# Kernel optimization log

Hardware: AMD Instinct MI355X
Metric: run time of the kernel (lower is better)

## Reference

```python
import jax, jax.numpy as jnp
import numpy as np

B, S, D = 2, 2048, 1024
H = 16
HD = D // H  # head dim 64


def setup_inputs() -> dict:
    key = jax.random.key(0)
    ks = jax.random.split(key, 7)
    queries = jax.random.normal(ks[0], (B, S, D), dtype=jnp.float32)
    keys = jax.random.normal(ks[1], (B, S, D), dtype=jnp.float32)
    values = jax.random.normal(ks[2], (B, S, D), dtype=jnp.float32)
    scale = 1.0 / np.sqrt(D)
    Wq = jax.random.normal(ks[3], (D, D), dtype=jnp.float32) * scale
    Wk = jax.random.normal(ks[4], (D, D), dtype=jnp.float32) * scale
    Wv = jax.random.normal(ks[5], (D, D), dtype=jnp.float32) * scale
    Wo = jax.random.normal(ks[6], (D, D), dtype=jnp.float32) * scale
    return {"queries": queries, "keys": keys, "values": values,
            "Wq": Wq, "Wk": Wk, "Wv": Wv, "Wo": Wo}


def _split_heads(x):
    # [B,S,D] -> [B,H,S,HD]
    b, s, d = x.shape
    return x.reshape(b, s, H, d // H).transpose(0, 2, 1, 3)


def reference(queries, keys, values, Wq, Wk, Wv, Wo):
    q = _split_heads(queries @ Wq) * (HD ** -0.5)   # [B,H,S,HD]
    k = _split_heads(keys @ Wk)
    v = _split_heads(values @ Wv)
    logits = jnp.einsum('bhqd,bhkd->bhqk', q, k)     # [B,H,S,S]
    weights = jax.nn.softmax(logits, axis=-1)
    ctx = jnp.einsum('bhqk,bhkd->bhqd', weights, v)  # [B,H,S,HD]
    ctx = ctx.transpose(0, 2, 1, 3).reshape(B, S, D)
    return ctx @ Wo
```

## Files before the change

### kernel.cpp

```cpp
#include <hip/hip_runtime.h>
#include <hip/hip_bf16.h>


typedef short s16x8 __attribute__((ext_vector_type(8)));
typedef float f32x4v __attribute__((ext_vector_type(4)));
typedef float f32x16v __attribute__((ext_vector_type(16)));
typedef unsigned int u32x4v __attribute__((ext_vector_type(4)));

__device__ inline unsigned short f2bf(float f) {
    union { float f; unsigned int i; } x; x.f = f;
    unsigned int r = x.i + 0x7FFFu + ((x.i >> 16) & 1u);
    return (unsigned short)(r >> 16);
}
__device__ inline unsigned int pkbf(float lo, float hi) {
    return (unsigned int)f2bf(lo) | ((unsigned int)f2bf(hi) << 16);
}

__device__ inline void gld_lds16(const unsigned short* g, unsigned short* l) {
    __builtin_amdgcn_global_load_lds(
        (const __attribute__((address_space(1))) unsigned int*)(const void*)g,
        (__attribute__((address_space(3))) unsigned int*)(void*)l,
        16, 0, 0);
}

__global__ __launch_bounds__(256)
void cvt3(const float* __restrict__ W0, const float* __restrict__ W1, const float* __restrict__ W2,
          unsigned short* __restrict__ T0, unsigned short* __restrict__ T1, unsigned short* __restrict__ T2) {
    const float* W = (blockIdx.z == 0) ? W0 : (blockIdx.z == 1) ? W1 : W2;
    unsigned short* Wt = (blockIdx.z == 0) ? T0 : (blockIdx.z == 1) ? T1 : T2;
    __shared__ __align__(16) unsigned short Ls[64 * 72];
    const int t = threadIdx.x;
    const int k0 = blockIdx.y * 64, n0 = blockIdx.x * 64;
    const int r = t >> 4, c4 = (t & 15) * 4;
    #pragma unroll
    for (int i = 0; i < 4; ++i) {
        float4 wv = *(const float4*)&W[(size_t)(k0 + r + i * 16) * 1024 + n0 + c4];
        Ls[(c4 + 0) * 72 + r + i * 16] = f2bf(wv.x);
        Ls[(c4 + 1) * 72 + r + i * 16] = f2bf(wv.y);
        Ls[(c4 + 2) * 72 + r + i * 16] = f2bf(wv.z);
        Ls[(c4 + 3) * 72 + r + i * 16] = f2bf(wv.w);
    }
    __syncthreads();
    #pragma unroll
    for (int i = 0; i < 2; ++i) {
        const int p = i * 256 + t;
        const int n = p & 63, kc = p >> 6;
        s16x8 v = *(const s16x8*)&Ls[n * 72 + kc * 8];
        const int gn = n0 + n, k = k0 + kc * 8;
        const size_t g = ((size_t)(gn >> 7) * 128 + (k >> 3)) * 128 + (gn & 127);
        *(s16x8*)&Wt[g * 8] = v;
    }
}

__global__ __launch_bounds__(256)
void cvtA(const float* __restrict__ A0, const float* __restrict__ A1, const float* __restrict__ A2,
          unsigned short* __restrict__ O0, unsigned short* __restrict__ O1, unsigned short* __restrict__ O2) {
    const float* A = (blockIdx.z == 0) ? A0 : (blockIdx.z == 1) ? A1 : A2;
    unsigned short* O = (blockIdx.z == 0) ? O0 : (blockIdx.z == 1) ? O1 : O2;
    __shared__ __align__(16) unsigned short Ls[8192];
    const int t = threadIdx.x;
    const int k0 = blockIdx.x * 64, rp = blockIdx.y;
    const int row = t >> 1, kh = (t & 1) * 32;
    const float* src = A + (size_t)(rp * 128 + row) * 1024 + k0 + kh;
    float4 f[8];
    #pragma unroll
    for (int i = 0; i < 8; ++i) f[i] = ((const float4*)src)[i];
    #pragma unroll
    for (int j = 0; j < 4; ++j) {
        uint4 u;
        u.x = pkbf(f[j * 2].x, f[j * 2].y);
        u.y = pkbf(f[j * 2].z, f[j * 2].w);
        u.z = pkbf(f[j * 2 + 1].x, f[j * 2 + 1].y);
        u.w = pkbf(f[j * 2 + 1].z, f[j * 2 + 1].w);
        const int kc = (t & 1) * 4 + j;
        *(uint4*)&Ls[(kc * 128 + row) * 8] = u;
    }
    __syncthreads();
    const size_t gbase = ((size_t)rp * 128 + (k0 >> 3)) * 128;
    #pragma unroll
    for (int i = 0; i < 4; ++i) {
        const int idx = i * 256 + t;
        *(uint4*)&O[(gbase + idx) * 8] = *(const uint4*)&Ls[idx * 8];
    }
}

__global__ __launch_bounds__(256, 3)
void gemm_qkv(const unsigned short* __restrict__ Aq, const unsigned short* __restrict__ Ak,
              const unsigned short* __restrict__ Av,
              const unsigned short* __restrict__ W0, const unsigned short* __restrict__ W1,
              const unsigned short* __restrict__ W2,
              unsigned short* __restrict__ OQ, unsigned short* __restrict__ OK,
              unsigned short* __restrict__ OV, float scaleQ) {
    const int p = blockIdx.x;
    const int L = (p & 7) * 96 + (p >> 3);
    const int z = L >> 8;
    const int rem = L & 255;
    const int m0 = (rem >> 3) * 128, n0 = (rem & 7) * 128;
    const unsigned short* Asw = (z == 0) ? Aq : (z == 1) ? Ak : Av;
    const unsigned short* Bsw = (z == 0) ? W0 : (z == 1) ? W1 : W2;
    const float scale = (z == 0) ? scaleQ : 1.0f;

    __shared__ __align__(16) unsigned short Al[2][4096];
    __shared__ __align__(16) unsigned short Bl[2][4096];
    const int t = threadIdx.x, lane = t & 63, w = t >> 6;
    const int ln = lane & 15, qd = lane >> 4;
    const int mw = (w & 1) * 64, nw = (w >> 1) * 64;
    const size_t gaB = (size_t)(m0 >> 7) * 16384;
    const size_t gbB = (size_t)(n0 >> 7) * 16384;

    f32x4v acc[4][4] = {};

    auto stage = [&](int kt, int b) {
        const size_t ga = gaB + (size_t)kt * 512;
        const size_t gb = gbB + (size_t)kt * 512;
        #pragma unroll
        for (int j = 0; j < 2; ++j)
            gld_lds16(Asw + (ga + j * 256 + t) * 8, &Al[b][(j * 256 + w * 64) * 8]);
        #pragma unroll
        for (int j = 0; j < 2; ++j)
            gld_lds16(Bsw + (gb + j * 256 + t) * 8, &Bl[b][(j * 256 + w * 64) * 8]);
    };

    stage(0, 0);
    stage(1, 1);
    for (int kt = 0; kt < 32; ++kt) {
        if (kt < 31) asm volatile("s_waitcnt vmcnt(4)" ::: "memory");
        else         asm volatile("s_waitcnt vmcnt(0)" ::: "memory");
        __builtin_amdgcn_s_barrier();
        asm volatile("" ::: "memory");
        const int b = kt & 1;
        {
            s16x8 a[4], bb[4];
            #pragma unroll
            for (int mt = 0; mt < 4; ++mt)
                a[mt] = *(const s16x8*)&Al[b][(qd * 128 + mw + mt * 16 + ln) * 8];
            #pragma unroll
            for (int nt = 0; nt < 4; ++nt)
                bb[nt] = *(const s16x8*)&Bl[b][(qd * 128 + nw + nt * 16 + ln) * 8];
            #pragma unroll
            for (int mt = 0; mt < 4; ++mt)
                #pragma unroll
                for (int nt = 0; nt < 4; ++nt)
                    acc[mt][nt] = __builtin_amdgcn_mfma_f32_16x16x32_bf16(a[mt], bb[nt], acc[mt][nt], 0, 0, 0);
        }
        if (kt < 30) {
            __builtin_amdgcn_s_barrier();
            asm volatile("" ::: "memory");
            stage(kt + 2, b);
        }
    }

    #pragma unroll
    for (int mt = 0; mt < 4; ++mt)
        #pragma unroll
        for (int nt = 0; nt < 4; ++nt)
            #pragma unroll
            for (int i = 0; i < 4; ++i) {
                const int m = m0 + mw + mt * 16 + qd * 4 + i;
                const int n = n0 + nw + nt * 16 + ln;
                const float v = acc[mt][nt][i] * scale;
                const int bh = (m >> 11) * 16 + (n >> 6), s = m & 2047, hd = n & 63;
                if (z == 0) {
                    OQ[((size_t)bh * 2048 + s) * 64 + hd] = f2bf(v);
                } else if (z == 1) {
                    const size_t g = ((size_t)(bh * 32 + (s >> 6)) * 8 + (hd >> 3)) * 64 + (s & 63);
                    OK[g * 8 + (hd & 7)] = f2bf(v);
                } else {
                    const size_t g = ((size_t)(bh * 32 + (s >> 6)) * 8 + ((s >> 3) & 7)) * 64 + hd;
                    OV[g * 8 + (s & 7)] = f2bf(v);
                }
            }
}

__global__ __launch_bounds__(256, 3)
void gemm_qkv_pack(const float* __restrict__ A0, const float* __restrict__ A1, const float* __restrict__ A2,
                   const unsigned short* __restrict__ W0, const unsigned short* __restrict__ W1,
                   const unsigned short* __restrict__ W2,
                   unsigned short* __restrict__ OQ, unsigned short* __restrict__ OK,
                   unsigned short* __restrict__ OV, float scaleQ) {
    const int z = blockIdx.z;
    const float* Avv = (z == 0) ? A0 : (z == 1) ? A1 : A2;
    const unsigned short* Bsw = (z == 0) ? W0 : (z == 1) ? W1 : W2;
    const float scale = (z == 0) ? scaleQ : 1.0f;

    __shared__ __align__(16) unsigned short Al[1024 * 8];
    __shared__ __align__(16) unsigned short Bl[1024 * 8];
    const int t = threadIdx.x;
    const int lane = t & 63, w = t >> 6;
    const int ln = lane & 15, qd = lane >> 4;
    const int mw = (w & 1) * 64, nw = (w >> 1) * 64;
    const int m0 = blockIdx.y * 128, n0 = blockIdx.x * 128;

    f32x4v acc[4][4] = {};

    for (int k0 = 0; k0 < 1024; k0 += 64) {
        __syncthreads();
        {
            const size_t gb = ((size_t)(n0 >> 7) * 128 + (k0 >> 3)) * 128;
            #pragma unroll
            for (int j = 0; j < 4; ++j)
                gld_lds16(Bsw + (gb + j * 256 + t) * 8, &Bl[(j * 256 + w * 64) * 8]);
        }
        #pragma unroll
        for (int j = 0; j < 4; ++j) {
            const int pp = j * 256 + t;
            const int row = pp >> 3, kc = pp & 7;
            const float* src = Avv + (size_t)(m0 + row) * 1024 + k0 + kc * 8;
            float4 f0 = ((const float4*)src)[0];
            float4 f1 = ((const float4*)src)[1];
            uint4 u;
            u.x = pkbf(f0.x, f0.y); u.y = pkbf(f0.z, f0.w);
            u.z = pkbf(f1.x, f1.y); u.w = pkbf(f1.z, f1.w);
            *(uint4*)&Al[(kc * 128 + (row ^ kc)) * 8] = u;
        }
        __syncthreads();

        #pragma unroll
        for (int kk = 0; kk < 2; ++kk) {
            const int kc = kk * 4 + qd;
            s16x8 a[4], b[4];
            #pragma unroll
            for (int mt = 0; mt < 4; ++mt)
                a[mt] = *(const s16x8*)&Al[(kc * 128 + ((mw + mt * 16 + ln) ^ kc)) * 8];
            #pragma unroll
            for (int nt = 0; nt < 4; ++nt)
                b[nt] = *(const s16x8*)&Bl[(kc * 128 + nw + nt * 16 + ln) * 8];
            #pragma unroll
            for (int mt = 0; mt < 4; ++mt)
                #pragma unroll
                for (int nt = 0; nt < 4; ++nt)
                    acc[mt][nt] = __builtin_amdgcn_mfma_f32_16x16x32_bf16(a[mt], b[nt], acc[mt][nt], 0, 0, 0);
        }
    }

    #pragma unroll
    for (int mt = 0; mt < 4; ++mt)
        #pragma unroll
        for (int nt = 0; nt < 4; ++nt)
            #pragma unroll
            for (int i = 0; i < 4; ++i) {
                const int m = m0 + mw + mt * 16 + qd * 4 + i;
                const int n = n0 + nw + nt * 16 + ln;
                const float v = acc[mt][nt][i] * scale;
                const int bh = (m >> 11) * 16 + (n >> 6), s = m & 2047, hd = n & 63;
                if (z == 0) {
                    OQ[((size_t)bh * 2048 + s) * 64 + hd] = f2bf(v);
                } else if (z == 1) {
                    const size_t g = ((size_t)(bh * 32 + (s >> 6)) * 8 + (hd >> 3)) * 64 + (s & 63);
                    OK[g * 8 + (hd & 7)] = f2bf(v);
                } else {
                    const size_t g = ((size_t)(bh * 32 + (s >> 6)) * 8 + ((s >> 3) & 7)) * 64 + hd;
                    OV[g * 8 + (s & 7)] = f2bf(v);
                }
            }
}

__global__ __launch_bounds__(256, 2)
void gemm_out(const unsigned short* __restrict__ Asw, const unsigned short* __restrict__ Bsw,
              float* __restrict__ outF) {
    const int p = blockIdx.x;
    const int L = (p & 7) * 64 + (p >> 3);
    const int m0 = (L >> 4) * 128, n0 = (L & 15) * 64;

    __shared__ __align__(16) unsigned short Al[2][8192];
    __shared__ __align__(16) unsigned short Bl[2][4096];
    const int t = threadIdx.x, lane = t & 63, w = t >> 6;
    const int ln = lane & 15, qd = lane >> 4;
    const int mw = (w & 1) * 64, nw = (w >> 1) * 32;
    const size_t gaB = (size_t)(m0 >> 7) * 16384;
    const size_t gbB = (size_t)(n0 >> 7) * 16384 + (n0 & 127);

    f32x4v acc[4][2] = {};

    auto stage = [&](int kt, int b) {
        const size_t ga = gaB + (size_t)kt * 1024;
        #pragma unroll
        for (int j = 0; j < 4; ++j)
            gld_lds16(Asw + (ga + j * 256 + t) * 8, &Al[b][(j * 256 + w * 64) * 8]);
        #pragma unroll
        for (int i = 0; i < 2; ++i) {
            const int c = w * 2 + i;
            const size_t gb = gbB + (size_t)(kt * 8 + c) * 128 + lane;
            gld_lds16(Bsw + gb * 8, &Bl[b][(c * 64) * 8]);
        }
    };

    stage(0, 0);
    stage(1, 1);
    for (int kt = 0; kt < 16; ++kt) {
        if (kt < 15) asm volatile("s_waitcnt vmcnt(6)" ::: "memory");
        else         asm volatile("s_waitcnt vmcnt(0)" ::: "memory");
        __builtin_amdgcn_s_barrier();
        asm volatile("" ::: "memory");
        const int b = kt & 1;
        #pragma unroll
        for (int kk = 0; kk < 2; ++kk) {
            const int kc = kk * 4 + qd;
            s16x8 a[4], bb[2];
            #pragma unroll
            for (int mt = 0; mt < 4; ++mt)
                a[mt] = *(const s16x8*)&Al[b][(kc * 128 + mw + mt * 16 + ln) * 8];
            #pragma unroll
            for (int nt = 0; nt < 2; ++nt)
                bb[nt] = *(const s16x8*)&Bl[b][(kc * 64 + nw + nt * 16 + ln) * 8];
            #pragma unroll
            for (int mt = 0; mt < 4; ++mt)
                #pragma unroll
                for (int nt = 0; nt < 2; ++nt)
                    acc[mt][nt] = __builtin_amdgcn_mfma_f32_16x16x32_bf16(a[mt], bb[nt], acc[mt][nt], 0, 0, 0);
        }
        if (kt < 14) {
            __builtin_amdgcn_s_barrier();
            asm volatile("" ::: "memory");
            stage(kt + 2, b);
        }
    }

    #pragma unroll
    for (int mt = 0; mt < 4; ++mt)
        #pragma unroll
        for (int nt = 0; nt < 2; ++nt)
            #pragma unroll
            for (int i = 0; i < 4; ++i) {
                const int m = m0 + mw + mt * 16 + qd * 4 + i;
                const int n = n0 + nw + nt * 16 + ln;
                outF[(size_t)m * 1024 + n] = acc[mt][nt][i];
            }
}

__device__ __forceinline__ void fa_compute(
        const unsigned short* Ksb, const unsigned short* Vsb,
        const int H, const int l31, const s16x8* qf,
        f32x16v* accO, float& ls0, float& ls1, float& ls2, float& ls3) {
    f32x16v accS[2] = {};
    #pragma unroll
    for (int kk = 0; kk < 4; ++kk) {
        s16x8 kf0 = *(const s16x8*)&Ksb[((kk * 2 + H) * 64 + l31) * 8];
        s16x8 kf1 = *(const s16x8*)&Ksb[((kk * 2 + H) * 64 + 32 + l31) * 8];
        accS[0] = __builtin_amdgcn_mfma_f32_32x32x16_bf16(kf0, qf[kk], accS[0], 0, 0, 0);
        accS[1] = __builtin_amdgcn_mfma_f32_32x32x16_bf16(kf1, qf[kk], accS[1], 0, 0, 0);
    }

    u32x4v af[4];
    #pragma unroll
    for (int mt = 0; mt < 2; ++mt) {
        float p[16];
        #pragma unroll
        for (int r = 0; r < 16; ++r)
            p[r] = exp2f(accS[mt][r]);
        #pragma unroll
        for (int r = 0; r < 16; r += 4) {
            ls0 += p[r + 0]; ls1 += p[r + 1]; ls2 += p[r + 2]; ls3 += p[r + 3];
        }
        unsigned int C[8];
        #pragma unroll
        for (int j = 0; j < 8; ++j)
            asm("v_cvt_pk_bf16_f32 %0, %1, %2" : "=v"(C[j]) : "v"(p[2 * j]), "v"(p[2 * j + 1]));
        #pragma unroll
        for (int pp = 0; pp < 2; ++pp) {
            unsigned int x0 = C[4 * pp + 0], y0 = C[4 * pp + 2];
            unsigned int x1 = C[4 * pp + 1], y1 = C[4 * pp + 3];
            asm("v_permlane32_swap_b32 %0, %1" : "+v"(x0), "+v"(y0));
            asm("v_permlane32_swap_b32 %0, %1" : "+v"(x1), "+v"(y1));
            u32x4v a; a.x = x0; a.y = x1; a.z = y0; a.w = y1;
            af[mt * 2 + pp] = a;
        }
    }

    #pragma unroll
    for (int kk2 = 0; kk2 < 4; ++kk2) {
        s16x8 a = __builtin_bit_cast(s16x8, af[kk2]);
        s16x8 vf0 = *(const s16x8*)&Vsb[((kk2 * 2 + H) * 64 + l31) * 8];
        s16x8 vf1 = *(const s16x8*)&Vsb[((kk2 * 2 + H) * 64 + 32 + l31) * 8];
        accO[0] = __builtin_amdgcn_mfma_f32_32x32x16_bf16(a, vf0, accO[0], 0, 0, 0);
        accO[1] = __builtin_amdgcn_mfma_f32_32x32x16_bf16(a, vf1, accO[1], 0, 0, 0);
    }
}

__global__ __launch_bounds__(256, 2)
void fattn(const unsigned short* __restrict__ Q, const unsigned short* __restrict__ Ksw,
           const unsigned short* __restrict__ Vsw, unsigned short* __restrict__ ctx) {
    __shared__ __align__(16) unsigned short Ks3[3][512 * 8];
    __shared__ __align__(16) unsigned short Vs3[3][512 * 8];

    const int t = threadIdx.x, lane = t & 63, w = t >> 6;
    const int l31 = lane & 31, H = lane >> 5;
    const int bid = blockIdx.x + (blockIdx.y << 4);
    const int wid = (bid & 7) * 64 + (bid >> 3);
    const int bh = wid >> 4, m0 = (wid & 15) * 128;
    const size_t head = (size_t)bh * 2048 * 64;

    s16x8 qf[4];
    #pragma unroll
    for (int kk = 0; kk < 4; ++kk)
        qf[kk] = *(const s16x8*)(Q + head + (size_t)(m0 + w * 32 + l31) * 64 + kk * 16 + H * 8);
    asm volatile("s_waitcnt vmcnt(0)" ::: "memory");
    #pragma unroll
    for (int kk = 0; kk < 4; ++kk) {
        u32x4v q = __builtin_bit_cast(u32x4v, qf[kk]);
        asm volatile("" : "+v"(q.x), "+v"(q.y), "+v"(q.z), "+v"(q.w));
        qf[kk] = __builtin_bit_cast(s16x8, q);
    }

    const size_t tb = (size_t)bh * 32 * 512;
    {
        #pragma unroll
        for (int kt = 0; kt < 2; ++kt)
            #pragma unroll
            for (int j = 0; j < 2; ++j) {
                gld_lds16(Ksw + (tb + kt * 512 + j * 256 + t) * 8, &Ks3[kt][(j * 256 + w * 64) * 8]);
                gld_lds16(Vsw + (tb + kt * 512 + j * 256 + t) * 8, &Vs3[kt][(j * 256 + w * 64) * 8]);
            }
    }

    f32x16v accO[2] = {};
    float ls0 = 0.f, ls1 = 0.f, ls2 = 0.f, ls3 = 0.f;

    int cur = 0;
    for (int kt = 0; kt < 31; ++kt) {
        asm volatile("s_waitcnt vmcnt(4)" ::: "memory");
        __builtin_amdgcn_s_barrier();
        asm volatile("" ::: "memory");
        if (kt < 30) {
            const int ib = (cur == 0) ? 2 : cur - 1;
            const size_t tbn = tb + (size_t)(kt + 2) * 512;
            #pragma unroll
            for (int j = 0; j < 2; ++j) {
                gld_lds16(Ksw + (tbn + j * 256 + t) * 8, &Ks3[ib][(j * 256 + w * 64) * 8]);
                gld_lds16(Vsw + (tbn + j * 256 + t) * 8, &Vs3[ib][(j * 256 + w * 64) * 8]);
            }
        }
        fa_compute(Ks3[cur], Vs3[cur], H, l31, qf, accO, ls0, ls1, ls2, ls3);
        cur = (cur == 2) ? 0 : cur + 1;
    }
    asm volatile("s_waitcnt vmcnt(0)" ::: "memory");
    __builtin_amdgcn_s_barrier();
    asm volatile("" ::: "memory");
    fa_compute(Ks3[cur], Vs3[cur], H, l31, qf, accO, ls0, ls1, ls2, ls3);

    float lsum = (ls0 + ls1) + (ls2 + ls3);
    lsum += __shfl_xor(lsum, 32, 64);
    const float inv = 1.f / lsum;

    #pragma unroll
    for (int r = 0; r < 16; ++r) {
        const int qloc = (r & 3) + 8 * (r >> 2) + 4 * H;
        const float rinv = __shfl(inv, qloc, 64);
        const int mrow = (bh >> 4) * 2048 + m0 + w * 32 + qloc;
        #pragma unroll
        for (int nt = 0; nt < 2; ++nt) {
            const int k = (bh & 15) * 64 + nt * 32 + l31;
            const size_t g = ((size_t)(mrow >> 7) * 128 + (k >> 3)) * 128 + (mrow & 127);
            ctx[g * 8 + (k & 7)] = f2bf(accO[nt][r] * rinv);
        }
    }
}

extern "C" void kernel_launch(void* const* d_in, const int* in_sizes, int n_in,
                              void* d_out, int out_size, void* d_ws, size_t ws_size,
                              hipStream_t stream) {
    char* ws = (char*)d_ws;
    unsigned short* Qb  = (unsigned short*)(ws);
    unsigned short* Ksw = (unsigned short*)(ws + ((size_t)8 << 20));
    unsigned short* Vsw = (unsigned short*)(ws + ((size_t)16 << 20));
    unsigned short* Wqt = (unsigned short*)(ws + ((size_t)24 << 20));
    unsigned short* Wkt = (unsigned short*)(ws + ((size_t)26 << 20));
    unsigned short* Wvt = (unsigned short*)(ws + ((size_t)28 << 20));
    unsigned short* Aq  = (unsigned short*)(ws + ((size_t)30 << 20));
    unsigned short* Ak  = (unsigned short*)(ws + ((size_t)38 << 20));
    unsigned short* Av  = (unsigned short*)(ws + ((size_t)46 << 20));
    unsigned short* ctx = (unsigned short*)(ws + ((size_t)24 << 20));
    unsigned short* Wot = (unsigned short*)(ws);

    const bool big = ws_size >= ((size_t)54 << 20);

    cvt3<<<dim3(16, 16, 3), 256, 0, stream>>>((const float*)d_in[3], (const float*)d_in[4],
                                              (const float*)d_in[5], Wqt, Wkt, Wvt);

    if (big) {
        cvtA<<<dim3(16, 32, 3), 256, 0, stream>>>((const float*)d_in[0], (const float*)d_in[1],
                                                  (const float*)d_in[2], Aq, Ak, Av);
        gemm_qkv<<<dim3(768), 256, 0, stream>>>(Aq, Ak, Av, Wqt, Wkt, Wvt,
                                                Qb, Ksw, Vsw, 0.125f * 1.44269504f);
    } else {
        gemm_qkv_pack<<<dim3(8, 32, 3), 256, 0, stream>>>(
            (const float*)d_in[0], (const float*)d_in[1], (const float*)d_in[2],
            Wqt, Wkt, Wvt, Qb, Ksw, Vsw, 0.125f * 1.44269504f);
    }

    fattn<<<dim3(16, 32), dim3(256), 0, stream>>>(Qb, Ksw, Vsw, ctx);

    cvt3<<<dim3(16, 16, 1), 256, 0, stream>>>((const float*)d_in[6], nullptr, nullptr,
                                              Wot, nullptr, nullptr);

    gemm_out<<<dim3(512), 256, 0, stream>>>(ctx, Wot, (float*)d_out);
}
```

Baseline: 233.0 us.

## Split attention over KV halves with combine kernel and MFMA row-sum

```diff
diff --git a/kernel.cpp b/kernel.cpp
--- a/kernel.cpp
+++ b/kernel.cpp
@@ -14,6 +14,9 @@
 }
 __device__ inline unsigned int pkbf(float lo, float hi) {
     return (unsigned int)f2bf(lo) | ((unsigned int)f2bf(hi) << 16);
+}
+__device__ inline float bf2f(unsigned short u) {
+    union { unsigned int i; float f; } x; x.i = (unsigned int)u << 16; return x.f;
 }
 
 __device__ inline void gld_lds16(const unsigned short* g, unsigned short* l) {
@@ -172,89 +175,6 @@
             }
 }
 
-__global__ __launch_bounds__(256, 3)
-void gemm_qkv_pack(const float* __restrict__ A0, const float* __restrict__ A1, const float* __restrict__ A2,
-                   const unsigned short* __restrict__ W0, const unsigned short* __restrict__ W1,
-                   const unsigned short* __restrict__ W2,
-                   unsigned short* __restrict__ OQ, unsigned short* __restrict__ OK,
-                   unsigned short* __restrict__ OV, float scaleQ) {
-    const int z = blockIdx.z;
-    const float* Avv = (z == 0) ? A0 : (z == 1) ? A1 : A2;
-    const unsigned short* Bsw = (z == 0) ? W0 : (z == 1) ? W1 : W2;
-    const float scale = (z == 0) ? scaleQ : 1.0f;
-
-    __shared__ __align__(16) unsigned short Al[1024 * 8];
-    __shared__ __align__(16) unsigned short Bl[1024 * 8];
-    const int t = threadIdx.x;
-    const int lane = t & 63, w = t >> 6;
-    const int ln = lane & 15, qd = lane >> 4;
-    const int mw = (w & 1) * 64, nw = (w >> 1) * 64;
-    const int m0 = blockIdx.y * 128, n0 = blockIdx.x * 128;
-
-    f32x4v acc[4][4] = {};
-
-    for (int k0 = 0; k0 < 1024; k0 += 64) {
-        __syncthreads();
-        {
-            const size_t gb = ((size_t)(n0 >> 7) * 128 + (k0 >> 3)) * 128;
-            #pragma unroll
-            for (int j = 0; j < 4; ++j)
-                gld_lds16(Bsw + (gb + j * 256 + t) * 8, &Bl[(j * 256 + w * 64) * 8]);
-        }
-        #pragma unroll
-        for (int j = 0; j < 4; ++j) {
-            const int pp = j * 256 + t;
-            const int row = pp >> 3, kc = pp & 7;
-            const float* src = Avv + (size_t)(m0 + row) * 1024 + k0 + kc * 8;
-            float4 f0 = ((const float4*)src)[0];
-            float4 f1 = ((const float4*)src)[1];
-            uint4 u;
-            u.x = pkbf(f0.x, f0.y); u.y = pkbf(f0.z, f0.w);
-            u.z = pkbf(f1.x, f1.y); u.w = pkbf(f1.z, f1.w);
-            *(uint4*)&Al[(kc * 128 + (row ^ kc)) * 8] = u;
-        }
-        __syncthreads();
-
-        #pragma unroll
-        for (int kk = 0; kk < 2; ++kk) {
-            const int kc = kk * 4 + qd;
-            s16x8 a[4], b[4];
-            #pragma unroll
-            for (int mt = 0; mt < 4; ++mt)
-                a[mt] = *(const s16x8*)&Al[(kc * 128 + ((mw + mt * 16 + ln) ^ kc)) * 8];
-            #pragma unroll
-            for (int nt = 0; nt < 4; ++nt)
-                b[nt] = *(const s16x8*)&Bl[(kc * 128 + nw + nt * 16 + ln) * 8];
-            #pragma unroll
-            for (int mt = 0; mt < 4; ++mt)
-                #pragma unroll
-                for (int nt = 0; nt < 4; ++nt)
-                    acc[mt][nt] = __builtin_amdgcn_mfma_f32_16x16x32_bf16(a[mt], b[nt], acc[mt][nt], 0, 0, 0);
-        }
-    }
-
-    #pragma unroll
-    for (int mt = 0; mt < 4; ++mt)
-        #pragma unroll
-        for (int nt = 0; nt < 4; ++nt)
-            #pragma unroll
-            for (int i = 0; i < 4; ++i) {
-                const int m = m0 + mw + mt * 16 + qd * 4 + i;
-                const int n = n0 + nw + nt * 16 + ln;
-                const float v = acc[mt][nt][i] * scale;
-                const int bh = (m >> 11) * 16 + (n >> 6), s = m & 2047, hd = n & 63;
-                if (z == 0) {
-                    OQ[((size_t)bh * 2048 + s) * 64 + hd] = f2bf(v);
-                } else if (z == 1) {
-                    const size_t g = ((size_t)(bh * 32 + (s >> 6)) * 8 + (hd >> 3)) * 64 + (s & 63);
-                    OK[g * 8 + (hd & 7)] = f2bf(v);
-                } else {
-                    const size_t g = ((size_t)(bh * 32 + (s >> 6)) * 8 + ((s >> 3) & 7)) * 64 + hd;
-                    OV[g * 8 + (s & 7)] = f2bf(v);
-                }
-            }
-}
-
 __global__ __launch_bounds__(256, 2)
 void gemm_out(const unsigned short* __restrict__ Asw, const unsigned short* __restrict__ Bsw,
               float* __restrict__ outF) {
@@ -331,7 +251,7 @@
 __device__ __forceinline__ void fa_compute(
         const unsigned short* Ksb, const unsigned short* Vsb,
         const int H, const int l31, const s16x8* qf,
-        f32x16v* accO, float& ls0, float& ls1, float& ls2, float& ls3) {
+        f32x16v* accO, f32x16v& accL) {
     f32x16v accS[2] = {};
     #pragma unroll
     for (int kk = 0; kk < 4; ++kk) {
@@ -348,10 +268,6 @@
         #pragma unroll
         for (int r = 0; r < 16; ++r)
             p[r] = exp2f(accS[mt][r]);
-        #pragma unroll
-        for (int r = 0; r < 16; r += 4) {
-            ls0 += p[r + 0]; ls1 += p[r + 1]; ls2 += p[r + 2]; ls3 += p[r + 3];
-        }
         unsigned int C[8];
         #pragma unroll
         for (int j = 0; j < 8; ++j)
@@ -367,6 +283,8 @@
         }
     }
 
+    const s16x8 ones = {(short)0x3F80, (short)0x3F80, (short)0x3F80, (short)0x3F80,
+                        (short)0x3F80, (short)0x3F80, (short)0x3F80, (short)0x3F80};
     #pragma unroll
     for (int kk2 = 0; kk2 < 4; ++kk2) {
         s16x8 a = __builtin_bit_cast(s16x8, af[kk2]);
@@ -374,20 +292,24 @@
         s16x8 vf1 = *(const s16x8*)&Vsb[((kk2 * 2 + H) * 64 + 32 + l31) * 8];
         accO[0] = __builtin_amdgcn_mfma_f32_32x32x16_bf16(a, vf0, accO[0], 0, 0, 0);
         accO[1] = __builtin_amdgcn_mfma_f32_32x32x16_bf16(a, vf1, accO[1], 0, 0, 0);
-    }
-}
-
-__global__ __launch_bounds__(256, 2)
-void fattn(const unsigned short* __restrict__ Q, const unsigned short* __restrict__ Ksw,
-           const unsigned short* __restrict__ Vsw, unsigned short* __restrict__ ctx) {
-    __shared__ __align__(16) unsigned short Ks3[3][512 * 8];
-    __shared__ __align__(16) unsigned short Vs3[3][512 * 8];
+        accL    = __builtin_amdgcn_mfma_f32_32x32x16_bf16(a, ones, accL, 0, 0, 0);
+    }
+}
+
+__global__ __launch_bounds__(256, 4)
+void fattn_sp(const unsigned short* __restrict__ Q, const unsigned short* __restrict__ Ksw,
+              const unsigned short* __restrict__ Vsw, unsigned short* __restrict__ Opart,
+              float* __restrict__ Lpart) {
+    __shared__ __align__(16) unsigned short Ks2[2][4096];
+    __shared__ __align__(16) unsigned short Vs2[2][4096];
 
     const int t = threadIdx.x, lane = t & 63, w = t >> 6;
     const int l31 = lane & 31, H = lane >> 5;
-    const int bid = blockIdx.x + (blockIdx.y << 4);
-    const int wid = (bid & 7) * 64 + (bid >> 3);
-    const int bh = wid >> 4, m0 = (wid & 15) * 128;
+    const int bid = blockIdx.x;
+    const int wid = (bid & 7) * 128 + (bid >> 3);
+    const int bh = wid >> 5, inner = wid & 31;
+    const int split = inner >> 4, mblk = inner & 15;
+    const int m0 = mblk * 128;
     const size_t head = (size_t)bh * 2048 * 64;
 
     s16x8 qf[4];
@@ -402,56 +324,96 @@
         qf[kk] = __builtin_bit_cast(s16x8, q);
     }
 
-    const size_t tb = (size_t)bh * 32 * 512;
-    {
-        #pragma unroll
-        for (int kt = 0; kt < 2; ++kt)
-            #pragma unroll
-            for (int j = 0; j < 2; ++j) {
-                gld_lds16(Ksw + (tb + kt * 512 + j * 256 + t) * 8, &Ks3[kt][(j * 256 + w * 64) * 8]);
-                gld_lds16(Vsw + (tb + kt * 512 + j * 256 + t) * 8, &Vs3[kt][(j * 256 + w * 64) * 8]);
-            }
-    }
+    const size_t tb = (size_t)(bh * 32 + split * 16) * 512;
+    auto stage = [&](int kt, int b) {
+        const size_t tk = tb + (size_t)kt * 512;
+        #pragma unroll
+        for (int j = 0; j < 2; ++j)
+            gld_lds16(Ksw + (tk + j * 256 + t) * 8, &Ks2[b][(j * 256 + w * 64) * 8]);
+        #pragma unroll
+        for (int j = 0; j < 2; ++j)
+            gld_lds16(Vsw + (tk + j * 256 + t) * 8, &Vs2[b][(j * 256 + w * 64) * 8]);
+    };
+
+    stage(0, 0);
+    stage(1, 1);
 
     f32x16v accO[2] = {};
-    float ls0 = 0.f, ls1 = 0.f, ls2 = 0.f, ls3 = 0.f;
-
-    int cur = 0;
-    for (int kt = 0; kt < 31; ++kt) {
-        asm volatile("s_waitcnt vmcnt(4)" ::: "memory");
+    f32x16v accL = {};
+
+    for (int kt = 0; kt < 16; ++kt) {
+        if (kt < 15) asm volatile("s_waitcnt vmcnt(4)" ::: "memory");
+        else         asm volatile("s_waitcnt vmcnt(0)" ::: "memory");
         __builtin_amdgcn_s_barrier();
         asm volatile("" ::: "memory");
-        if (kt < 30) {
-            const int ib = (cur == 0) ? 2 : cur - 1;
-            const size_t tbn = tb + (size_t)(kt + 2) * 512;
-            #pragma unroll
-            for (int j = 0; j < 2; ++j) {
-                gld_lds16(Ksw + (tbn + j * 256 + t) * 8, &Ks3[ib][(j * 256 + w * 64) * 8]);
-                gld_lds16(Vsw + (tbn + j * 256 + t) * 8, &Vs3[ib][(j * 256 + w * 64) * 8]);
-            }
-        }
-        fa_compute(Ks3[cur], Vs3[cur], H, l31, qf, accO, ls0, ls1, ls2, ls3);
-        cur = (cur == 2) ? 0 : cur + 1;
-    }
-    asm volatile("s_waitcnt vmcnt(0)" ::: "memory");
-    __builtin_amdgcn_s_barrier();
-    asm volatile("" ::: "memory");
-    fa_compute(Ks3[cur], Vs3[cur], H, l31, qf, accO, ls0, ls1, ls2, ls3);
-
-    float lsum = (ls0 + ls1) + (ls2 + ls3);
-    lsum += __shfl_xor(lsum, 32, 64);
-    const float inv = 1.f / lsum;
+        fa_compute(Ks2[kt & 1], Vs2[kt & 1], H, l31, qf, accO, accL);
+        if (kt < 14) {
+            __builtin_amdgcn_s_barrier();
+            asm volatile("" ::: "memory");
+            stage(kt + 2, kt & 1);
+        }
+    }
+
+    const int lb = bh * 16 + mblk;
+    unsigned int Wd[16];
+    #pragma unroll
+    for (int nt = 0; nt < 2; ++nt)
+        #pragma unroll
+        for (int r = 0; r < 16; r += 2)
+            Wd[nt * 8 + r / 2] = pkbf(accO[nt][r], accO[nt][r + 1]);
+    uint4* od = (uint4*)(Opart + ((size_t)(split * 512 + lb) * 256 + t) * 32);
+    od[0] = *(const uint4*)&Wd[0];
+    od[1] = *(const uint4*)&Wd[4];
+    od[2] = *(const uint4*)&Wd[8];
+    od[3] = *(const uint4*)&Wd[12];
+    if (l31 == 0) {
+        float lv[16];
+        #pragma unroll
+        for (int r = 0; r < 16; ++r) lv[r] = accL[r];
+        float4* ld = (float4*)(Lpart + (((size_t)(split * 512 + lb) * 4 + w) * 2 + H) * 16);
+        ld[0] = *(const float4*)&lv[0];
+        ld[1] = *(const float4*)&lv[4];
+        ld[2] = *(const float4*)&lv[8];
+        ld[3] = *(const float4*)&lv[12];
+    }
+}
+
+__global__ __launch_bounds__(256)
+void fa_comb(const unsigned short* __restrict__ Opart, const float* __restrict__ Lpart,
+             unsigned short* __restrict__ ctx) {
+    const int lb = blockIdx.x, t = threadIdx.x;
+    const int lane = t & 63, w = t >> 6;
+    const int l31 = lane & 31, H = lane >> 5;
+    const int bh = lb >> 4, m0 = (lb & 15) * 128;
+
+    const float* L0 = Lpart + (((size_t)lb * 4 + w) * 2 + H) * 16;
+    const float* L1 = Lpart + (((size_t)(512 + lb) * 4 + w) * 2 + H) * 16;
+    float inv[16];
+    #pragma unroll
+    for (int r = 0; r < 16; ++r) inv[r] = 1.f / (L0[r] + L1[r]);
+
+    const uint4* o0 = (const uint4*)(Opart + ((size_t)lb * 256 + t) * 32);
+    const uint4* o1 = (const uint4*)(Opart + ((size_t)(512 + lb) * 256 + t) * 32);
+    unsigned int A0[16], A1[16];
+    *(uint4*)&A0[0] = o0[0]; *(uint4*)&A0[4] = o0[1];
+    *(uint4*)&A0[8] = o0[2]; *(uint4*)&A0[12] = o0[3];
+    *(uint4*)&A1[0] = o1[0]; *(uint4*)&A1[4] = o1[1];
+    *(uint4*)&A1[8] = o1[2]; *(uint4*)&A1[12] = o1[3];
 
     #pragma unroll
     for (int r = 0; r < 16; ++r) {
         const int qloc = (r & 3) + 8 * (r >> 2) + 4 * H;
-        const float rinv = __shfl(inv, qloc, 64);
         const int mrow = (bh >> 4) * 2048 + m0 + w * 32 + qloc;
         #pragma unroll
         for (int nt = 0; nt < 2; ++nt) {
+            const int j = nt * 16 + r;
+            const unsigned int w0 = A0[j >> 1], w1 = A1[j >> 1];
+            const unsigned short h0 = (j & 1) ? (unsigned short)(w0 >> 16) : (unsigned short)(w0 & 0xFFFF);
+            const unsigned short h1 = (j & 1) ? (unsigned short)(w1 >> 16) : (unsigned short)(w1 & 0xFFFF);
+            const float out = (bf2f(h0) + bf2f(h1)) * inv[r];
             const int k = (bh & 15) * 64 + nt * 32 + l31;
             const size_t g = ((size_t)(mrow >> 7) * 128 + (k >> 3)) * 128 + (mrow & 127);
-            ctx[g * 8 + (k & 7)] = f2bf(accO[nt][r] * rinv);
+            ctx[g * 8 + (k & 7)] = f2bf(out);
         }
     }
 }
@@ -460,35 +422,30 @@
                               void* d_out, int out_size, void* d_ws, size_t ws_size,
                               hipStream_t stream) {
     char* ws = (char*)d_ws;
-    unsigned short* Qb  = (unsigned short*)(ws);
-    unsigned short* Ksw = (unsigned short*)(ws + ((size_t)8 << 20));
-    unsigned short* Vsw = (unsigned short*)(ws + ((size_t)16 << 20));
-    unsigned short* Wqt = (unsigned short*)(ws + ((size_t)24 << 20));
-    unsigned short* Wkt = (unsigned short*)(ws + ((size_t)26 << 20));
-    unsigned short* Wvt = (unsigned short*)(ws + ((size_t)28 << 20));
-    unsigned short* Aq  = (unsigned short*)(ws + ((size_t)30 << 20));
-    unsigned short* Ak  = (unsigned short*)(ws + ((size_t)38 << 20));
-    unsigned short* Av  = (unsigned short*)(ws + ((size_t)46 << 20));
-    unsigned short* ctx = (unsigned short*)(ws + ((size_t)24 << 20));
-    unsigned short* Wot = (unsigned short*)(ws);
-
-    const bool big = ws_size >= ((size_t)54 << 20);
+    unsigned short* Qb    = (unsigned short*)(ws);
+    unsigned short* Ksw   = (unsigned short*)(ws + ((size_t)8 << 20));
+    unsigned short* Vsw   = (unsigned short*)(ws + ((size_t)16 << 20));
+    unsigned short* Wqt   = (unsigned short*)(ws + ((size_t)24 << 20));
+    unsigned short* Wkt   = (unsigned short*)(ws + ((size_t)26 << 20));
+    unsigned short* Wvt   = (unsigned short*)(ws + ((size_t)28 << 20));
+    unsigned short* Aq    = (unsigned short*)(ws + ((size_t)30 << 20));
+    unsigned short* Ak    = (unsigned short*)(ws + ((size_t)38 << 20));
+    unsigned short* Av    = (unsigned short*)(ws + ((size_t)46 << 20));
+    unsigned short* ctx   = (unsigned short*)(ws + ((size_t)24 << 20));
+    unsigned short* Opart = (unsigned short*)(ws + ((size_t)32 << 20));
+    float*          Lpart = (float*)         (ws + ((size_t)48 << 20));
+    unsigned short* Wot   = (unsigned short*)(ws);
 
     cvt3<<<dim3(16, 16, 3), 256, 0, stream>>>((const float*)d_in[3], (const float*)d_in[4],
                                               (const float*)d_in[5], Wqt, Wkt, Wvt);
 
-    if (big) {
-        cvtA<<<dim3(16, 32, 3), 256, 0, stream>>>((const float*)d_in[0], (const float*)d_in[1],
-                                                  (const float*)d_in[2], Aq, Ak, Av);
-        gemm_qkv<<<dim3(768), 256, 0, stream>>>(Aq, Ak, Av, Wqt, Wkt, Wvt,
-                                                Qb, Ksw, Vsw, 0.125f * 1.44269504f);
-    } else {
-        gemm_qkv_pack<<<dim3(8, 32, 3), 256, 0, stream>>>(
-            (const float*)d_in[0], (const float*)d_in[1], (const float*)d_in[2],
-            Wqt, Wkt, Wvt, Qb, Ksw, Vsw, 0.125f * 1.44269504f);
-    }
-
-    fattn<<<dim3(16, 32), dim3(256), 0, stream>>>(Qb, Ksw, Vsw, ctx);
+    cvtA<<<dim3(16, 32, 3), 256, 0, stream>>>((const float*)d_in[0], (const float*)d_in[1],
+                                              (const float*)d_in[2], Aq, Ak, Av);
+    gemm_qkv<<<dim3(768), 256, 0, stream>>>(Aq, Ak, Av, Wqt, Wkt, Wvt,
+                                            Qb, Ksw, Vsw, 0.125f * 1.44269504f);
+
+    fattn_sp<<<dim3(1024), 256, 0, stream>>>(Qb, Ksw, Vsw, Opart, Lpart);
+    fa_comb<<<dim3(512), 256, 0, stream>>>(Opart, Lpart, ctx);
 
     cvt3<<<dim3(16, 16, 1), 256, 0, stream>>>((const float*)d_in[6], nullptr, nullptr,
                                               Wot, nullptr, nullptr);
```

Result: faster. 225.7 us (-3.1%).
